# Performance work log

Hardware: AMD Instinct MI355X
Metric: run time of the kernel (lower is better)

Reference implementation:

```python
import jax, jax.numpy as jnp
import numpy as np

N = 100000
E = 3200000
HOP = 10

def setup_inputs() -> dict:
    key = jax.random.key(0)
    ks = jax.random.split(key, 10)
    n_in, n_hid, n_out = 512, 256, 64
    x = jax.random.normal(ks[0], (N, n_in), dtype=jnp.float32)
    edge_row = jax.random.randint(ks[1], (E,), 0, N, dtype=jnp.int32)
    edge_col = jax.random.randint(ks[2], (E,), 0, N, dtype=jnp.int32)
    # row-normalized-ish positive edge values (like a transition matrix)
    edge_vals = jax.random.uniform(ks[3], (E,), dtype=jnp.float32) / 32.0
    A2 = jax.random.uniform(ks[4], (N, 1), dtype=jnp.float32)
    # xavier-ish init scaled down for numerical sanity
    W1 = jax.random.normal(ks[5], (n_in, n_hid), dtype=jnp.float32) * (2.0 / (n_in + n_hid)) ** 0.5
    b1 = jnp.zeros((n_hid,), dtype=jnp.float32)
    W3 = jax.random.normal(ks[6], (n_hid, n_hid), dtype=jnp.float32) * (2.0 / (2 * n_hid)) ** 0.5
    b3 = jnp.zeros((n_hid,), dtype=jnp.float32)
    W2 = jax.random.normal(ks[7], (n_hid, n_out), dtype=jnp.float32) * (2.0 / (n_hid + n_out)) ** 0.5
    b2 = jnp.zeros((n_out,), dtype=jnp.float32)
    return {"x": x, "edge_row": edge_row, "edge_col": edge_col, "edge_vals": edge_vals,
            "A2": A2, "W1": W1, "b1": b1, "W3": W3, "b3": b3, "W2": W2, "b2": b2}

def _spmm(edge_row, edge_col, edge_vals, h):
    # sparse [N,N] @ dense [N,F] via gather + segment_sum
    msgs = edge_vals[:, None] * h[edge_col]          # [E, F]
    return jax.ops.segment_sum(msgs, edge_row, num_segments=N)

def reference(x, edge_row, edge_col, edge_vals, A2, W1, b1, W3, b3, W2, b2):
    # dropout layers are identity at eval time
    x0 = jax.nn.relu(x @ W1 + b1)                    # [N, n_hid]
    h = x0
    for _ in range(HOP):
        h = _spmm(edge_row, edge_col, edge_vals, h) + A2 * x0
        h = jax.nn.relu(h + h @ W3 + b3)
    return h @ W2 + b2                               # [N, n_out]
```

## Files before the change

kernel.cpp:

```cpp
#include <hip/hip_runtime.h>
#include <stdint.h>


typedef unsigned short bf16_t;
typedef __attribute__((ext_vector_type(8))) short bf16x8;
typedef __attribute__((ext_vector_type(8))) unsigned short u16x8;
typedef __attribute__((ext_vector_type(4))) float f32x4;

__device__ __forceinline__ float bf2f(bf16_t u) {
    union { unsigned int i; float f; } v; v.i = ((unsigned int)u) << 16; return v.f;
}
__device__ __forceinline__ bf16_t f2bf(float f) {
    union { float f; unsigned int i; } v; v.f = f;
    unsigned int x = v.i;
    unsigned int r = (x + 0x7fffu + ((x >> 16) & 1u)) >> 16;
    return (bf16_t)r;
}

__global__ void zero_i32(int* __restrict__ p, int n) {
    int i = blockIdx.x * blockDim.x + threadIdx.x;
    if (i < n) p[i] = 0;
}

__global__ void transpose_w(const float* __restrict__ W, bf16_t* __restrict__ Wt,
                            int K, int N) {
    int i = blockIdx.x * blockDim.x + threadIdx.x;
    if (i < K * N) {
        int k = i / N, n = i % N;
        Wt[(size_t)n * K + k] = f2bf(W[i]);
    }
}

__global__ void count_edges(const int* __restrict__ er, int* __restrict__ cnt,
                            int E, int N) {
    int i = blockIdx.x * blockDim.x + threadIdx.x;
    if (i < E) {
        unsigned r = (unsigned)er[i];
        if (r < (unsigned)N) atomicAdd(&cnt[r], 1);
    }
}

__global__ __launch_bounds__(1024)
void scan_rows(int* cnt_cursor, int* __restrict__ row_ptr, int n) {
    __shared__ int sums[1024];
    int t = threadIdx.x;
    int chunk = (n + 1023) >> 10;
    int start = t * chunk;
    int end = min(start + chunk, n);
    int s = 0;
    for (int i = start; i < end; ++i) s += cnt_cursor[i];
    sums[t] = s;
    __syncthreads();
    for (int off = 1; off < 1024; off <<= 1) {
        int v = (t >= off) ? sums[t - off] : 0;
        __syncthreads();
        sums[t] += v;
        __syncthreads();
    }
    int run = (t == 0) ? 0 : sums[t - 1];
    for (int i = start; i < end; ++i) {
        int c = cnt_cursor[i];
        row_ptr[i] = run;
        run += c;
    }
    if (t == 1023) row_ptr[n] = sums[1023];
}

__global__ void init_bcur(const int* __restrict__ row_ptr, int* __restrict__ bcur,
                          int N, int NB) {
    int b = blockIdx.x * blockDim.x + threadIdx.x;
    if (b < NB) bcur[b] = row_ptr[min(b << 8, N)];
}

#define BIN_CHUNK 8192
#define NBMAX 392
__global__ __launch_bounds__(256)
void bin_edges(const int* __restrict__ er, const int* __restrict__ ec,
               const float* __restrict__ ev, int* __restrict__ bcur,
               int2* __restrict__ binned, int E, int N, int NB) {
    __shared__ int cnt[NBMAX];
    __shared__ int resv[NBMAX];
    int tid = threadIdx.x;
    int e0 = blockIdx.x * BIN_CHUNK;
    int n = min(BIN_CHUNK, E - e0);
    for (int b = tid; b < NB; b += 256) cnt[b] = 0;
    __syncthreads();
    for (int i = tid; i < n; i += 256) {
        unsigned r = (unsigned)er[e0 + i];
        if (r < (unsigned)N) atomicAdd(&cnt[r >> 8], 1);
    }
    __syncthreads();
    for (int b = tid; b < NB; b += 256) {
        int c = cnt[b];
        resv[b] = c ? atomicAdd(&bcur[b], c) : 0;
        cnt[b] = 0;
    }
    __syncthreads();
    for (int i = tid; i < n; i += 256) {
        unsigned r = (unsigned)er[e0 + i];
        if (r < (unsigned)N) {
            unsigned c = (unsigned)ec[e0 + i];
            float v = ev[e0 + i];
            if (c >= (unsigned)N) { c = 0; v = 0.f; }
            int b = (int)(r >> 8);
            int p = resv[b] + atomicAdd(&cnt[b], 1);
            binned[p] = make_int2((int)(((r & 255u) << 17) | c), __float_as_int(v));
        }
    }
}

#define BCAP 9216
__global__ __launch_bounds__(256)
void bucket_sort(const int* __restrict__ row_ptr, int2* __restrict__ csr, int N) {
    __shared__ int2 ent[BCAP];
    __shared__ int cnt[256];
    __shared__ int base[256];
    __shared__ int lcur[256];
    int b = blockIdx.x;
    int tid = threadIdx.x;
    int r0 = b << 8;
    int e0 = row_ptr[r0];
    int e1 = row_ptr[min(r0 + 256, N)];
    int n = e1 - e0;
    cnt[tid] = 0;
    __syncthreads();
    for (int i = tid; i < n; i += 256) {
        int2 p = csr[e0 + i];
        if (i < BCAP) ent[i] = p;
        atomicAdd(&cnt[((unsigned)p.x >> 17) & 255u], 1);
    }
    __syncthreads();
    int v0 = cnt[tid];
    for (int off = 1; off < 256; off <<= 1) {
        int u = (tid >= off) ? cnt[tid - off] : 0;
        __syncthreads();
        cnt[tid] += u;
        __syncthreads();
    }
    base[tid] = cnt[tid] - v0;
    lcur[tid] = 0;
    __syncthreads();
    for (int i = tid; i < n; i += 256) {
        int2 p = (i < BCAP) ? ent[i] : csr[e0 + i];
        int rl = (int)(((unsigned)p.x >> 17) & 255u);
        int d = base[rl] + atomicAdd(&lcur[rl], 1);
        csr[e0 + d] = make_int2(p.x & 0x1FFFF, p.y);
    }
}

__device__ __forceinline__ void fma8(float* acc, float v, u16x8 hv) {
    #pragma unroll
    for (int k = 0; k < 8; ++k)
        acc[k] = fmaf(v, bf2f((bf16_t)hv[k]), acc[k]);
}

__global__ __launch_bounds__(512, 4)
void fused_hop(const int* __restrict__ row_ptr, const int2* __restrict__ csr,
               const bf16_t* __restrict__ hin, const bf16_t* __restrict__ x0,
               const float* __restrict__ A2, const bf16_t* __restrict__ W3t,
               const float* __restrict__ bias, bf16_t* __restrict__ hout, int M) {
    __shared__ bf16_t s_tile[128 * 256];
    __shared__ bf16_t Bs[256 * 32];
    const int tid = threadIdx.x;
    const int w = tid >> 6, lane = tid & 63;
    const int bm = blockIdx.x * 128;
    const int half = lane >> 5, l32 = lane & 31, fo = l32 << 3;

    for (int rr = 0; rr < 16; ++rr) {
        int lrow = w * 16 + rr;
        int row = bm + lrow;
        float acc[8];
        #pragma unroll
        for (int k = 0; k < 8; ++k) acc[k] = 0.f;
        if (row < M) {
            if (half == 0) {
                float a2 = A2[row];
                u16x8 xv = *(const u16x8*)&x0[(row << 8) + fo];
                #pragma unroll
                for (int k = 0; k < 8; ++k) acc[k] = a2 * bf2f((bf16_t)xv[k]);
            }
            int e = row_ptr[row], e1 = row_ptr[row + 1];
            int nb = (e1 - e) >> 3;
            int2 q0, q1, q2, q3;
            if (nb > 0) {
                int eb = e + half;
                q0 = csr[eb]; q1 = csr[eb + 2]; q2 = csr[eb + 4]; q3 = csr[eb + 6];
            }
            for (int b = 0; b < nb; ++b) {
                int2 p0 = q0, p1 = q1, p2 = q2, p3 = q3;
                if (b + 1 < nb) {
                    int eb = e + 8 + half;
                    q0 = csr[eb]; q1 = csr[eb + 2]; q2 = csr[eb + 4]; q3 = csr[eb + 6];
                }
                u16x8 h0 = *(const u16x8*)&hin[(p0.x << 8) + fo];
                u16x8 h1 = *(const u16x8*)&hin[(p1.x << 8) + fo];
                u16x8 h2 = *(const u16x8*)&hin[(p2.x << 8) + fo];
                u16x8 h3 = *(const u16x8*)&hin[(p3.x << 8) + fo];
                fma8(acc, __int_as_float(p0.y), h0);
                fma8(acc, __int_as_float(p1.y), h1);
                fma8(acc, __int_as_float(p2.y), h2);
                fma8(acc, __int_as_float(p3.y), h3);
                e += 8;
            }
            for (; e + 2 <= e1; e += 2) {
                int2 p = csr[e + half];
                u16x8 hv = *(const u16x8*)&hin[(p.x << 8) + fo];
                fma8(acc, __int_as_float(p.y), hv);
            }
            if (e < e1 && half == 0) {
                int2 p = csr[e];
                u16x8 hv = *(const u16x8*)&hin[(p.x << 8) + fo];
                fma8(acc, __int_as_float(p.y), hv);
            }
            #pragma unroll
            for (int k = 0; k < 8; ++k) acc[k] += __shfl_xor(acc[k], 32, 64);
        }
        if (half == 0) {
            u16x8 o;
            #pragma unroll
            for (int k = 0; k < 8; ++k) o[k] = f2bf(acc[k]);
            *(u16x8*)((char*)s_tile + lrow * 512 + (((fo << 1)) ^ ((lrow & 7) << 4))) = o;
        }
    }
    __syncthreads();

    const int q = lane >> 4, l16 = lane & 15;
    const int wm = (w & 1) * 64, wn = (w >> 1) * 64;
    f32x4 acc2[4][4] = {};
    for (int k0 = 0; k0 < 256; k0 += 32) {
        #pragma unroll
        for (int r = 0; r < 2; ++r) {
            int rowbase = r * 128 + w * 16;
            int row = rowbase + (lane >> 2);
            const bf16_t* gp = W3t + (size_t)row * 256 + k0 + (lane & 3) * 8;
            bf16_t* lp = Bs + rowbase * 32 + lane * 8;
            __builtin_amdgcn_global_load_lds(
                (const __attribute__((address_space(1))) unsigned int*)gp,
                (__attribute__((address_space(3))) unsigned int*)lp, 16, 0, 0);
        }
        __syncthreads();
        bf16x8 afr[4], bfr[4];
        #pragma unroll
        for (int ms = 0; ms < 4; ++ms) {
            int ar = wm + ms * 16 + l16;
            afr[ms] = *(const bf16x8*)((const char*)s_tile + ar * 512 +
                       ((((k0 + q * 8) << 1)) ^ ((ar & 7) << 4)));
        }
        #pragma unroll
        for (int ns = 0; ns < 4; ++ns)
            bfr[ns] = *(const bf16x8*)&Bs[(wn + ns * 16 + l16) * 32 + q * 8];
        #pragma unroll
        for (int ms = 0; ms < 4; ++ms)
            #pragma unroll
            for (int ns = 0; ns < 4; ++ns)
                acc2[ms][ns] = __builtin_amdgcn_mfma_f32_16x16x32_bf16(
                    afr[ms], bfr[ns], acc2[ms][ns], 0, 0, 0);
        __syncthreads();
    }

    #pragma unroll
    for (int ms = 0; ms < 4; ++ms) {
        #pragma unroll
        for (int r = 0; r < 4; ++r) {
            int lrow = wm + ms * 16 + q * 4 + r;
            int grow = bm + lrow;
            if (grow < M) {
                #pragma unroll
                for (int ns = 0; ns < 4; ++ns) {
                    int col = wn + ns * 16 + l16;
                    float v = acc2[ms][ns][r] + bias[col];
                    v += bf2f(*(const bf16_t*)((const char*)s_tile + lrow * 512 +
                              (((col << 1)) ^ ((lrow & 7) << 4))));
                    v = fmaxf(v, 0.f);
                    hout[(size_t)grow * 256 + col] = f2bf(v);
                }
            }
        }
    }
}

template <int WM, int WN, bool AF32, bool RELU, typename CT>
__global__ __launch_bounds__(256)
void mfma_gemm(const void* __restrict__ Av, const bf16_t* __restrict__ Bt,
               const float* __restrict__ bias, CT* __restrict__ C,
               int M, int K, int Nfull) {
    constexpr int TM = WM * 64;
    constexpr int TN = WN * 64;
    __shared__ bf16_t As[TM * 32];
    __shared__ bf16_t Bs[TN * 32];
    const int tid = threadIdx.x;
    const int w = tid >> 6, lane = tid & 63;
    const int q = lane >> 4, l16 = lane & 15;
    const int bm = blockIdx.x * TM;
    const int bn = blockIdx.y * TN;
    const int wm = (w % WM) * 64;
    const int wn = (w / WM) * 64;

    f32x4 acc[4][4] = {};

    for (int k0 = 0; k0 < K; k0 += 32) {
        if constexpr (AF32) {
            constexpr int TPR = 256 / TM;
            constexpr int EPT = TM / 8;
            const float* A = (const float*)Av;
            int row = tid / TPR;
            int gr = min(bm + row, M - 1);
            int off = (tid % TPR) * EPT;
            const float* src = A + (size_t)gr * K + k0 + off;
            bf16_t* dst = As + row * 32 + off;
            #pragma unroll
            for (int g = 0; g < EPT / 4; ++g) {
                float4 v = *(const float4*)(src + 4 * g);
                ushort4 u;
                u.x = f2bf(v.x); u.y = f2bf(v.y); u.z = f2bf(v.z); u.w = f2bf(v.w);
                *(ushort4*)(dst + 4 * g) = u;
            }
        } else {
            const bf16_t* A = (const bf16_t*)Av;
            #pragma unroll
            for (int r = 0; r < TM / 64; ++r) {
                int rowbase = r * 64 + w * 16;
                int row = rowbase + (lane >> 2);
                int gr = min(bm + row, M - 1);
                const bf16_t* gp = A + (size_t)gr * K + k0 + (lane & 3) * 8;
                bf16_t* lp = As + rowbase * 32 + lane * 8;
                __builtin_amdgcn_global_load_lds(
                    (const __attribute__((address_space(1))) unsigned int*)gp,
                    (__attribute__((address_space(3))) unsigned int*)lp, 16, 0, 0);
            }
        }
        #pragma unroll
        for (int r = 0; r < TN / 64; ++r) {
            int rowbase = r * 64 + w * 16;
            int row = rowbase + (lane >> 2);
            const bf16_t* gp = Bt + (size_t)(bn + row) * K + k0 + (lane & 3) * 8;
            bf16_t* lp = Bs + rowbase * 32 + lane * 8;
            __builtin_amdgcn_global_load_lds(
                (const __attribute__((address_space(1))) unsigned int*)gp,
                (__attribute__((address_space(3))) unsigned int*)lp, 16, 0, 0);
        }
        __syncthreads();

        bf16x8 afr[4], bfr[4];
        #pragma unroll
        for (int ms = 0; ms < 4; ++ms)
            afr[ms] = *(const bf16x8*)&As[(wm + ms * 16 + l16) * 32 + q * 8];
        #pragma unroll
        for (int ns = 0; ns < 4; ++ns)
            bfr[ns] = *(const bf16x8*)&Bs[(wn + ns * 16 + l16) * 32 + q * 8];
        #pragma unroll
        for (int ms = 0; ms < 4; ++ms)
            #pragma unroll
            for (int ns = 0; ns < 4; ++ns)
                acc[ms][ns] = __builtin_amdgcn_mfma_f32_16x16x32_bf16(
                    afr[ms], bfr[ns], acc[ms][ns], 0, 0, 0);
        __syncthreads();
    }

    #pragma unroll
    for (int ms = 0; ms < 4; ++ms) {
        #pragma unroll
        for (int r = 0; r < 4; ++r) {
            int row = bm + wm + ms * 16 + q * 4 + r;
            if (row < M) {
                #pragma unroll
                for (int ns = 0; ns < 4; ++ns) {
                    int col = bn + wn + ns * 16 + l16;
                    float v = acc[ms][ns][r] + bias[col];
                    if constexpr (RELU) v = fmaxf(v, 0.f);
                    if constexpr (sizeof(CT) == 2) C[(size_t)row * Nfull + col] = (CT)f2bf(v);
                    else                           C[(size_t)row * Nfull + col] = (CT)v;
                }
            }
        }
    }
}

extern "C" void kernel_launch(void* const* d_in, const int* in_sizes, int n_in,
                              void* d_out, int out_size, void* d_ws, size_t ws_size,
                              hipStream_t stream) {
    const float* x   = (const float*)d_in[0];
    const int* erow  = (const int*)d_in[1];
    const int* ecol  = (const int*)d_in[2];
    const float* ev  = (const float*)d_in[3];
    const float* A2  = (const float*)d_in[4];
    const float* W1  = (const float*)d_in[5];
    const float* b1  = (const float*)d_in[6];
    const float* W3  = (const float*)d_in[7];
    const float* b3  = (const float*)d_in[8];
    const float* W2  = (const float*)d_in[9];
    const float* b2  = (const float*)d_in[10];
    float* out = (float*)d_out;

    const int N   = in_sizes[4];
    const int E   = in_sizes[1];
    const int NIN = in_sizes[0] / N;
    const int NH  = in_sizes[6];
    const int NO  = in_sizes[10];
    if (NH != 256 || NIN != 512 || NO != 64) return;
    const int NB = (N + 255) >> 8;
    if (NB > NBMAX) return;

    char* ws = (char*)d_ws;
    size_t off = 0;
    auto alloc = [&](size_t bytes) -> void* {
        void* p = ws + off;
        off += (bytes + 255) & ~(size_t)255;
        return p;
    };
    bf16_t* x0     = (bf16_t*)alloc((size_t)N * NH * 2);
    bf16_t* hA     = (bf16_t*)alloc((size_t)N * NH * 2);
    bf16_t* hB     = (bf16_t*)alloc((size_t)N * NH * 2);
    int*   row_ptr = (int*)alloc((size_t)(N + 1) * 4);
    int*   counts  = (int*)alloc((size_t)N * 4);
    int*   bcur    = (int*)alloc((size_t)NB * 4);
    int2*  csr     = (int2*)alloc((size_t)E * 8);
    bf16_t* W1t    = (bf16_t*)alloc((size_t)NIN * NH * 2);
    bf16_t* W3t    = (bf16_t*)alloc((size_t)NH * NH * 2);
    bf16_t* W2t    = (bf16_t*)alloc((size_t)NH * NO * 2);
    if (off > ws_size) return;

    zero_i32<<<(N + 255) / 256, 256, 0, stream>>>(counts, N);
    count_edges<<<(E + 255) / 256, 256, 0, stream>>>(erow, counts, E, N);
    scan_rows<<<1, 1024, 0, stream>>>(counts, row_ptr, N);
    init_bcur<<<(NB + 255) / 256, 256, 0, stream>>>(row_ptr, bcur, N, NB);
    bin_edges<<<(E + BIN_CHUNK - 1) / BIN_CHUNK, 256, 0, stream>>>(
        erow, ecol, ev, bcur, csr, E, N, NB);
    bucket_sort<<<NB, 256, 0, stream>>>(row_ptr, csr, N);
    transpose_w<<<(NIN * NH + 255) / 256, 256, 0, stream>>>(W1, W1t, NIN, NH);
    transpose_w<<<(NH * NH + 255) / 256, 256, 0, stream>>>(W3, W3t, NH, NH);
    transpose_w<<<(NH * NO + 255) / 256, 256, 0, stream>>>(W2, W2t, NH, NO);

    dim3 g1((N + 63) / 64, 1);
    mfma_gemm<1, 4, true, true, bf16_t><<<g1, 256, 0, stream>>>(
        x, W1t, b1, x0, N, NIN, NH);

    const bf16_t* hin = x0;
    bf16_t* hout = hA;
    for (int hop = 0; hop < 10; ++hop) {
        fused_hop<<<(N + 127) / 128, 512, 0, stream>>>(
            row_ptr, csr, hin, x0, A2, W3t, b3, hout, N);
        hin = hout;
        hout = (hout == hA) ? hB : hA;
    }

    dim3 g2((N + 255) / 256, 1);
    mfma_gemm<4, 1, false, false, float><<<g2, 256, 0, stream>>>(
        (const void*)hin, W2t, b2, out, N, NH, NO);
}
```

Measured before the change: 3.367 ms.

## Halve fused hop row tile and build row pointers from bucket counts

The fused SpMM+GEMM hop kernel now processes 64 rows per block instead of 128. That halves its shared-memory tile, raises the launch-bounds occupancy hint from 4 to 6 blocks, and gives more blocks for load balance on the latency-bound gather. CSR construction drops the per-row atomic count and the single-block 100K-element scan. It now counts per 256-row bucket, scans about 400 buckets, and derives row_ptr inside bucket_sort from the local histogram. The trade-off is that the W3 tile is reloaded twice as often per row and each wave does less MFMA work.

```diff
diff --git a/kernel.cpp b/kernel.cpp
--- a/kernel.cpp
+++ b/kernel.cpp
@@ -31,49 +31,51 @@
     }
 }
 
-__global__ void count_edges(const int* __restrict__ er, int* __restrict__ cnt,
-                            int E, int N) {
-    int i = blockIdx.x * blockDim.x + threadIdx.x;
-    if (i < E) {
-        unsigned r = (unsigned)er[i];
-        if (r < (unsigned)N) atomicAdd(&cnt[r], 1);
-    }
-}
-
-__global__ __launch_bounds__(1024)
-void scan_rows(int* cnt_cursor, int* __restrict__ row_ptr, int n) {
-    __shared__ int sums[1024];
-    int t = threadIdx.x;
-    int chunk = (n + 1023) >> 10;
-    int start = t * chunk;
-    int end = min(start + chunk, n);
-    int s = 0;
-    for (int i = start; i < end; ++i) s += cnt_cursor[i];
-    sums[t] = s;
-    __syncthreads();
-    for (int off = 1; off < 1024; off <<= 1) {
-        int v = (t >= off) ? sums[t - off] : 0;
-        __syncthreads();
-        sums[t] += v;
-        __syncthreads();
-    }
-    int run = (t == 0) ? 0 : sums[t - 1];
-    for (int i = start; i < end; ++i) {
-        int c = cnt_cursor[i];
-        row_ptr[i] = run;
-        run += c;
-    }
-    if (t == 1023) row_ptr[n] = sums[1023];
-}
-
-__global__ void init_bcur(const int* __restrict__ row_ptr, int* __restrict__ bcur,
-                          int N, int NB) {
-    int b = blockIdx.x * blockDim.x + threadIdx.x;
-    if (b < NB) bcur[b] = row_ptr[min(b << 8, N)];
-}
-
 #define BIN_CHUNK 8192
 #define NBMAX 392
+
+__global__ __launch_bounds__(256)
+void bin_count(const int* __restrict__ er, int* __restrict__ bcnt, int E, int N,
+               int NB) {
+    __shared__ int cnt[NBMAX];
+    int tid = threadIdx.x;
+    for (int b = tid; b < NB; b += 256) cnt[b] = 0;
+    __syncthreads();
+    int e0 = blockIdx.x * BIN_CHUNK;
+    int n = min(BIN_CHUNK, E - e0);
+    for (int i = tid; i < n; i += 256) {
+        unsigned r = (unsigned)er[e0 + i];
+        if (r < (unsigned)N) atomicAdd(&cnt[r >> 8], 1);
+    }
+    __syncthreads();
+    for (int b = tid; b < NB; b += 256) {
+        int c = cnt[b];
+        if (c) atomicAdd(&bcnt[b], c);
+    }
+}
+
+__global__ __launch_bounds__(512)
+void scan_buckets(const int* __restrict__ bcnt, int* __restrict__ bucket_base,
+                  int* __restrict__ bcur, int NB) {
+    __shared__ int s[512];
+    int t = threadIdx.x;
+    int v = (t < NB) ? bcnt[t] : 0;
+    s[t] = v;
+    __syncthreads();
+    for (int off = 1; off < 512; off <<= 1) {
+        int u = (t >= off) ? s[t - off] : 0;
+        __syncthreads();
+        s[t] += u;
+        __syncthreads();
+    }
+    if (t < NB) {
+        int excl = s[t] - v;
+        bucket_base[t] = excl;
+        bcur[t] = excl;
+        if (t == NB - 1) bucket_base[NB] = s[t];
+    }
+}
+
 __global__ __launch_bounds__(256)
 void bin_edges(const int* __restrict__ er, const int* __restrict__ ec,
                const float* __restrict__ ev, int* __restrict__ bcur,
@@ -111,7 +113,8 @@
 
 #define BCAP 9216
 __global__ __launch_bounds__(256)
-void bucket_sort(const int* __restrict__ row_ptr, int2* __restrict__ csr, int N) {
+void bucket_sort(const int* __restrict__ bucket_base, int2* __restrict__ csr,
+                 int* __restrict__ row_ptr, int N, int NB) {
     __shared__ int2 ent[BCAP];
     __shared__ int cnt[256];
     __shared__ int base[256];
@@ -119,8 +122,8 @@
     int b = blockIdx.x;
     int tid = threadIdx.x;
     int r0 = b << 8;
-    int e0 = row_ptr[r0];
-    int e1 = row_ptr[min(r0 + 256, N)];
+    int e0 = bucket_base[b];
+    int e1 = bucket_base[b + 1];
     int n = e1 - e0;
     cnt[tid] = 0;
     __syncthreads();
@@ -139,6 +142,8 @@
     }
     base[tid] = cnt[tid] - v0;
     lcur[tid] = 0;
+    if (r0 + tid < N) row_ptr[r0 + tid] = e0 + cnt[tid] - v0;
+    if (b == NB - 1 && tid == 255) row_ptr[N] = e1;
     __syncthreads();
     for (int i = tid; i < n; i += 256) {
         int2 p = (i < BCAP) ? ent[i] : csr[e0 + i];
@@ -154,20 +159,20 @@
         acc[k] = fmaf(v, bf2f((bf16_t)hv[k]), acc[k]);
 }
 
-__global__ __launch_bounds__(512, 4)
+__global__ __launch_bounds__(512, 6)
 void fused_hop(const int* __restrict__ row_ptr, const int2* __restrict__ csr,
                const bf16_t* __restrict__ hin, const bf16_t* __restrict__ x0,
                const float* __restrict__ A2, const bf16_t* __restrict__ W3t,
                const float* __restrict__ bias, bf16_t* __restrict__ hout, int M) {
-    __shared__ bf16_t s_tile[128 * 256];
+    __shared__ bf16_t s_tile[64 * 256];
     __shared__ bf16_t Bs[256 * 32];
     const int tid = threadIdx.x;
     const int w = tid >> 6, lane = tid & 63;
-    const int bm = blockIdx.x * 128;
+    const int bm = blockIdx.x * 64;
     const int half = lane >> 5, l32 = lane & 31, fo = l32 << 3;
 
-    for (int rr = 0; rr < 16; ++rr) {
-        int lrow = w * 16 + rr;
+    for (int rr = 0; rr < 8; ++rr) {
+        int lrow = w * 8 + rr;
         int row = bm + lrow;
         float acc[8];
         #pragma unroll
@@ -219,14 +224,14 @@
             u16x8 o;
             #pragma unroll
             for (int k = 0; k < 8; ++k) o[k] = f2bf(acc[k]);
-            *(u16x8*)((char*)s_tile + lrow * 512 + (((fo << 1)) ^ ((lrow & 7) << 4))) = o;
+            *(u16x8*)((char*)s_tile + lrow * 512 + ((fo << 1) ^ ((lrow & 7) << 4))) = o;
         }
     }
     __syncthreads();
 
     const int q = lane >> 4, l16 = lane & 15;
-    const int wm = (w & 1) * 64, wn = (w >> 1) * 64;
-    f32x4 acc2[4][4] = {};
+    const int wm = (w & 1) * 32, wn = (w >> 1) * 64;
+    f32x4 acc2[2][4] = {};
     for (int k0 = 0; k0 < 256; k0 += 32) {
         #pragma unroll
         for (int r = 0; r < 2; ++r) {
@@ -239,18 +244,18 @@
                 (__attribute__((address_space(3))) unsigned int*)lp, 16, 0, 0);
         }
         __syncthreads();
-        bf16x8 afr[4], bfr[4];
-        #pragma unroll
-        for (int ms = 0; ms < 4; ++ms) {
+        bf16x8 afr[2], bfr[4];
+        #pragma unroll
+        for (int ms = 0; ms < 2; ++ms) {
             int ar = wm + ms * 16 + l16;
             afr[ms] = *(const bf16x8*)((const char*)s_tile + ar * 512 +
-                       ((((k0 + q * 8) << 1)) ^ ((ar & 7) << 4)));
+                       (((k0 + q * 8) << 1) ^ ((ar & 7) << 4)));
         }
         #pragma unroll
         for (int ns = 0; ns < 4; ++ns)
             bfr[ns] = *(const bf16x8*)&Bs[(wn + ns * 16 + l16) * 32 + q * 8];
         #pragma unroll
-        for (int ms = 0; ms < 4; ++ms)
+        for (int ms = 0; ms < 2; ++ms)
             #pragma unroll
             for (int ns = 0; ns < 4; ++ns)
                 acc2[ms][ns] = __builtin_amdgcn_mfma_f32_16x16x32_bf16(
@@ -259,7 +264,7 @@
     }
 
     #pragma unroll
-    for (int ms = 0; ms < 4; ++ms) {
+    for (int ms = 0; ms < 2; ++ms) {
         #pragma unroll
         for (int r = 0; r < 4; ++r) {
             int lrow = wm + ms * 16 + q * 4 + r;
@@ -270,7 +275,7 @@
                     int col = wn + ns * 16 + l16;
                     float v = acc2[ms][ns][r] + bias[col];
                     v += bf2f(*(const bf16_t*)((const char*)s_tile + lrow * 512 +
-                              (((col << 1)) ^ ((lrow & 7) << 4))));
+                              ((col << 1) ^ ((lrow & 7) << 4))));
                     v = fmaxf(v, 0.f);
                     hout[(size_t)grow * 256 + col] = f2bf(v);
                 }
@@ -412,7 +417,8 @@
     bf16_t* hA     = (bf16_t*)alloc((size_t)N * NH * 2);
     bf16_t* hB     = (bf16_t*)alloc((size_t)N * NH * 2);
     int*   row_ptr = (int*)alloc((size_t)(N + 1) * 4);
-    int*   counts  = (int*)alloc((size_t)N * 4);
+    int*   bcnt    = (int*)alloc((size_t)NB * 4);
+    int*   bbase   = (int*)alloc((size_t)(NB + 1) * 4);
     int*   bcur    = (int*)alloc((size_t)NB * 4);
     int2*  csr     = (int2*)alloc((size_t)E * 8);
     bf16_t* W1t    = (bf16_t*)alloc((size_t)NIN * NH * 2);
@@ -420,13 +426,13 @@
     bf16_t* W2t    = (bf16_t*)alloc((size_t)NH * NO * 2);
     if (off > ws_size) return;
 
-    zero_i32<<<(N + 255) / 256, 256, 0, stream>>>(counts, N);
-    count_edges<<<(E + 255) / 256, 256, 0, stream>>>(erow, counts, E, N);
-    scan_rows<<<1, 1024, 0, stream>>>(counts, row_ptr, N);
-    init_bcur<<<(NB + 255) / 256, 256, 0, stream>>>(row_ptr, bcur, N, NB);
+    zero_i32<<<1, 512, 0, stream>>>(bcnt, NB);
+    bin_count<<<(E + BIN_CHUNK - 1) / BIN_CHUNK, 256, 0, stream>>>(
+        erow, bcnt, E, N, NB);
+    scan_buckets<<<1, 512, 0, stream>>>(bcnt, bbase, bcur, NB);
     bin_edges<<<(E + BIN_CHUNK - 1) / BIN_CHUNK, 256, 0, stream>>>(
         erow, ecol, ev, bcur, csr, E, N, NB);
-    bucket_sort<<<NB, 256, 0, stream>>>(row_ptr, csr, N);
+    bucket_sort<<<NB, 256, 0, stream>>>(bbase, csr, row_ptr, N, NB);
     transpose_w<<<(NIN * NH + 255) / 256, 256, 0, stream>>>(W1, W1t, NIN, NH);
     transpose_w<<<(NH * NH + 255) / 256, 256, 0, stream>>>(W3, W3t, NH, NH);
     transpose_w<<<(NH * NO + 255) / 256, 256, 0, stream>>>(W2, W2t, NH, NO);
@@ -438,7 +444,7 @@
     const bf16_t* hin = x0;
     bf16_t* hout = hA;
     for (int hop = 0; hop < 10; ++hop) {
-        fused_hop<<<(N + 127) / 128, 512, 0, stream>>>(
+        fused_hop<<<(N + 63) / 64, 512, 0, stream>>>(
             row_ptr, csr, hin, x0, A2, W3t, b3, hout, N);
         hin = hout;
         hout = (hout == hA) ? hB : hA;
```

Measured after the change: 3.092 ms. 8.1% less time.
